# Optimization experiments

Hardware: AMD Instinct MI355X
Metric: run time of the kernel (lower is better)

The kernel has to match this reference:

```python
import jax, jax.numpy as jnp
import numpy as np

EMBED_DIM = 1024
HEAD_SIZE = 64
B, T = 4, 4096


def setup_inputs() -> dict:
    key = jax.random.key(0)
    kx, kq, kk, kv = jax.random.split(key, 4)
    x = jax.random.normal(kx, (B, T, EMBED_DIM), dtype=jnp.float32)
    sw = 1.0 / np.sqrt(EMBED_DIM)  # kaiming-ish init scale for linear weights
    Wq = jax.random.normal(kq, (EMBED_DIM, HEAD_SIZE), dtype=jnp.float32) * sw
    Wk = jax.random.normal(kk, (EMBED_DIM, HEAD_SIZE), dtype=jnp.float32) * sw
    Wv = jax.random.normal(kv, (EMBED_DIM, HEAD_SIZE), dtype=jnp.float32) * sw
    return {"x": x, "Wq": Wq, "Wk": Wk, "Wv": Wv}


def reference(x, Wq, Wk, Wv):
    Bn, Tn, C = x.shape
    q = jnp.einsum('btc,ch->bth', x, Wq)
    k = jnp.einsum('btc,ch->bth', x, Wk)
    v = jnp.einsum('btc,ch->bth', x, Wv)
    # NOTE: original scales by sqrt(C) = sqrt(embed_dim), not sqrt(head_size)
    scale = 1.0 / jnp.sqrt(jnp.asarray(C, dtype=x.dtype))
    wei = jnp.einsum('bth,bsh->bts', q, k) * scale  # [B, T, T]
    causal = jnp.tril(jnp.ones((Tn, Tn), dtype=bool))
    wei = jnp.where(causal, wei, -jnp.inf)
    wei = jax.nn.softmax(wei, axis=-1)
    # dropout p=0.0 (eval mode): identity
    return jnp.einsum('bts,bsh->bth', wei, v)
```

## Files before the change

### kernel.cpp

```cpp
#include <hip/hip_runtime.h>
#include <cstdint>


typedef __bf16 bf16;
typedef __bf16 bf16x4 __attribute__((ext_vector_type(4)));
typedef __bf16 bf16x8 __attribute__((ext_vector_type(8)));
typedef float  f32x4  __attribute__((ext_vector_type(4)));

#define MFMA16(a, b, c) __builtin_amdgcn_mfma_f32_16x16x32_bf16((a), (b), (c), 0, 0, 0)

#if __has_builtin(__builtin_amdgcn_exp2f)
#define EXP2(x) __builtin_amdgcn_exp2f(x)
#else
#define EXP2(x) exp2f(x)
#endif

#define B_SZ 4
#define T_SZ 4096
#define C_SZ 1024
#define H_SZ 64
#define M_SZ (B_SZ * T_SZ)
#define QSCALE (1.4426950408889634f / 32.0f)
#define P_O 8192
#define P_L 128

__device__ __forceinline__ void dma16(const void* g, void* l) {
    __builtin_amdgcn_global_load_lds(
        (const __attribute__((address_space(1))) uint32_t*)(uintptr_t)g,
        (__attribute__((address_space(3))) uint32_t*)(uint32_t)(uintptr_t)l,
        16, 0, 0);
}

__device__ __forceinline__ void pipe_sync() {
    asm volatile("s_waitcnt vmcnt(0)" ::: "memory");
    __builtin_amdgcn_s_barrier();
    __builtin_amdgcn_sched_barrier(0);
}

__global__ __launch_bounds__(256) void wt_prep(
    const float* __restrict__ Wq, const float* __restrict__ Wk,
    const float* __restrict__ Wv, bf16* __restrict__ wt2)
{
    const int n4 = blockIdx.x, t = threadIdx.x;
    const int nbase = n4 * 4;
    const float* W = (nbase < 64) ? Wq : (nbase < 128 ? Wk : Wv);
    const float sc = (nbase < 64) ? QSCALE : 1.0f;
    const int ncol = nbase & 63;
    #pragma unroll
    for (int i = 0; i < 4; ++i) {
        const int k = i * 256 + t;
        const float4 v = *(const float4*)(W + (size_t)k * H_SZ + ncol);
        const float vals[4] = {v.x, v.y, v.z, v.w};
        const size_t base = (size_t)(k >> 6) * 12288 + (size_t)((k >> 5) & 1) * 6144
                          + (size_t)((k >> 3) & 3) * 1536 + (k & 7);
        #pragma unroll
        for (int m = 0; m < 4; ++m)
            wt2[base + (size_t)(nbase + m) * 8] = (bf16)(vals[m] * sc);
    }
}

__global__ __launch_bounds__(256) void qkv_proj(
    const float* __restrict__ x, const bf16* __restrict__ wt2,
    bf16* __restrict__ qw, bf16* __restrict__ kw2, bf16* __restrict__ vtw2)
{
    const int m0 = blockIdx.x * 32;
    const int tid = threadIdx.x;
    const int wave = tid >> 6, lane = tid & 63;
    const int quad = lane >> 4, l15 = lane & 15;
    const int phase = blockIdx.x & 15;

    __shared__ __align__(16) float xs[2 * 4 * 32 * 8];
    __shared__ __align__(16) bf16  ws[2 * 4 * 192 * 8];

    f32x4 acc[2][3] = {};

    const char* xg = (const char*)x
        + (size_t)(m0 + ((tid >> 1) & 31)) * 4096
        + (size_t)((tid >> 6) & 3) * 32 + (size_t)(tid & 1) * 16;
    char* xl = (char*)xs + (size_t)tid * 16;
    const char* wg = (const char*)wt2 + (size_t)tid * 16;
    char* wl = (char*)ws + (size_t)tid * 16;

    for (int s = 0; s < 16; ++s) {
        const size_t se = (size_t)((s + phase) & 15);
        __syncthreads();
        dma16(xg + se * 256, xl);
        dma16(xg + se * 256 + 128, xl + 4096);
        #pragma unroll
        for (int i = 0; i < 6; ++i)
            dma16(wg + se * 24576 + (size_t)i * 4096, wl + (size_t)i * 4096);
        __syncthreads();

        #pragma unroll
        for (int ss = 0; ss < 2; ++ss) {
            bf16x8 a[2];
            #pragma unroll
            for (int mg = 0; mg < 2; ++mg) {
                const float* ap = xs + ss * 1024 + quad * 256 + (mg * 16 + l15) * 8;
                const f32x4 lo = *(const f32x4*)ap;
                const f32x4 hi = *(const f32x4*)(ap + 4);
                a[mg][0] = (bf16)lo[0]; a[mg][1] = (bf16)lo[1];
                a[mg][2] = (bf16)lo[2]; a[mg][3] = (bf16)lo[3];
                a[mg][4] = (bf16)hi[0]; a[mg][5] = (bf16)hi[1];
                a[mg][6] = (bf16)hi[2]; a[mg][7] = (bf16)hi[3];
            }
            #pragma unroll
            for (int i = 0; i < 3; ++i) {
                const int nt = wave * 3 + i;
                const bf16x8 wf = *(const bf16x8*)(ws + ss * 6144 + quad * 1536
                                                   + (nt * 16 + l15) * 8);
                #pragma unroll
                for (int mg = 0; mg < 2; ++mg)
                    acc[mg][i] = MFMA16(a[mg], wf, acc[mg][i]);
            }
        }
    }

    #pragma unroll
    for (int mg = 0; mg < 2; ++mg)
        #pragma unroll
        for (int i = 0; i < 3; ++i) {
            const int n = (wave * 3 + i) * 16 + l15;
            const int which = n >> 6, col = n & 63;
            #pragma unroll
            for (int r = 0; r < 4; ++r) {
                const int t = m0 + mg * 16 + quad * 4 + r;
                const bf16 v = (bf16)acc[mg][i][r];
                if (which == 0) {
                    qw[(size_t)t * H_SZ + col] = v;
                } else if (which == 1) {
                    kw2[(size_t)(t >> 6) * 4096
                        + (size_t)(((col >> 5) << 2) + ((col >> 3) & 3)) * 512
                        + (size_t)(t & 63) * 8 + (col & 7)] = v;
                } else {
                    const int t6 = t & 63;
                    const int p = ((t6 >> 2) & 3) * 8 + (t6 & 3) * 2
                                + ((t6 >> 4) & 1) + (t6 >> 5) * 32;
                    vtw2[(size_t)(t >> 6) * 4096
                         + (size_t)(p >> 3) * 512 + (size_t)col * 8 + (p & 7)] = v;
                }
            }
        }
}

__global__ __launch_bounds__(256) void flash_attn(
    const bf16* __restrict__ qw, const bf16* __restrict__ kw2,
    const bf16* __restrict__ vtw2, bf16* __restrict__ pbuf_o,
    float* __restrict__ pbuf_l)
{
    const int bx = blockIdx.x;
    const int item = (bx & 1) ? (511 - (bx >> 1)) : (bx >> 1);
    const int qt2 = 31 - (item >> 4);
    const int b   = (item >> 2) & 3;
    const int h   = item & 3;
    const int i0  = qt2 * 128;
    const int nkv = qt2 * 2 + 2;

    const int tid = threadIdx.x;
    const int wave = tid >> 6, lane = tid & 63;
    const int quad = lane >> 4, l15 = lane & 15;

    __shared__ __align__(16) bf16 kvs[2][8192];

    bf16x8 aq[2][2];
    #pragma unroll
    for (int mg2 = 0; mg2 < 2; ++mg2) {
        const bf16* qp = qw + ((size_t)b * T_SZ + i0 + wave * 32 + mg2 * 16 + l15) * H_SZ
                       + quad * 8;
        aq[mg2][0] = *(const bf16x8*)qp;
        aq[mg2][1] = *(const bf16x8*)(qp + 32);
    }
    const bf16 onev = (bf16)1.0f;
    const bf16x8 vone = {onev, onev, onev, onev, onev, onev, onev, onev};

    const char* kgb = (const char*)kw2 + (size_t)b * 524288;
    const char* vgb = (const char*)vtw2 + (size_t)b * 524288;

    f32x4 o[2][4] = {};
    f32x4 osum[2] = {};

    auto stage = [&](int jt, int buf) {
        const char* ks = kgb + (size_t)jt * 8192;
        const char* vs = vgb + (size_t)jt * 8192;
        char* dst = (char*)(&kvs[buf][0]) + (size_t)tid * 16;
        dma16(ks + (size_t)tid * 16, dst);
        dma16(ks + 4096 + (size_t)tid * 16, dst + 4096);
        dma16(vs + (size_t)tid * 16, dst + 8192);
        dma16(vs + 4096 + (size_t)tid * 16, dst + 12288);
    };

    if (h < nkv) {
        stage(h, 0);
        pipe_sync();
    }

    int c = 0;
    for (int jt = h; jt < nkv; jt += 4, c ^= 1) {
        if (jt + 4 < nkv) stage(jt + 4, c ^ 1);
        const bf16* kb = &kvs[c][0];
        const bf16* vb = &kvs[c][0] + 4096;

        f32x4 s4t[4][2] = {};
        __builtin_amdgcn_s_setprio(1);
        #pragma unroll
        for (int ct = 0; ct < 4; ++ct) {
            const bf16x8 k0 = *(const bf16x8*)(kb + (0 * 4 + quad) * 512 + (ct * 16 + l15) * 8);
            const bf16x8 k1 = *(const bf16x8*)(kb + (1 * 4 + quad) * 512 + (ct * 16 + l15) * 8);
            #pragma unroll
            for (int mg2 = 0; mg2 < 2; ++mg2) {
                s4t[ct][mg2] = MFMA16(k0, aq[mg2][0], s4t[ct][mg2]);
                s4t[ct][mg2] = MFMA16(k1, aq[mg2][1], s4t[ct][mg2]);
            }
        }
        __builtin_amdgcn_s_setprio(0);

        if (jt >= 2 * qt2) {
            #pragma unroll
            for (int mg2 = 0; mg2 < 2; ++mg2) {
                const int gq = i0 + wave * 32 + mg2 * 16 + l15;
                #pragma unroll
                for (int ct = 0; ct < 4; ++ct) {
                    const int gkv0 = jt * 64 + ct * 16 + quad * 4;
                    #pragma unroll
                    for (int rr = 0; rr < 4; ++rr)
                        if (gkv0 + rr > gq) s4t[ct][mg2][rr] = -3.0e38f;
                }
            }
        }

        bf16x8 pa[2][2];
        #pragma unroll
        for (int mg2 = 0; mg2 < 2; ++mg2)
            #pragma unroll
            for (int j = 0; j < 8; ++j) {
                pa[mg2][0][j] = (bf16)EXP2(s4t[j & 1][mg2][j >> 1]);
                pa[mg2][1][j] = (bf16)EXP2(s4t[2 + (j & 1)][mg2][j >> 1]);
            }

        __builtin_amdgcn_s_setprio(1);
        #pragma unroll
        for (int ht = 0; ht < 4; ++ht) {
            const bf16x8 v0 = *(const bf16x8*)(vb + (0 * 4 + quad) * 512 + (ht * 16 + l15) * 8);
            const bf16x8 v1 = *(const bf16x8*)(vb + (1 * 4 + quad) * 512 + (ht * 16 + l15) * 8);
            #pragma unroll
            for (int mg2 = 0; mg2 < 2; ++mg2) {
                o[mg2][ht] = MFMA16(pa[mg2][0], v0, o[mg2][ht]);
                o[mg2][ht] = MFMA16(pa[mg2][1], v1, o[mg2][ht]);
            }
        }
        #pragma unroll
        for (int mg2 = 0; mg2 < 2; ++mg2) {
            osum[mg2] = MFMA16(pa[mg2][0], vone, osum[mg2]);
            osum[mg2] = MFMA16(pa[mg2][1], vone, osum[mg2]);
        }
        __builtin_amdgcn_s_setprio(0);

        pipe_sync();
    }

    bf16* pb_o = pbuf_o + (size_t)(((b * 32 + qt2) * 4) + h) * P_O;
    float* pb_l = pbuf_l + (size_t)(((b * 32 + qt2) * 4) + h) * P_L;
    #pragma unroll
    for (int mg2 = 0; mg2 < 2; ++mg2) {
        const int L0 = wave * 32 + mg2 * 16 + quad * 4;
        #pragma unroll
        for (int ht = 0; ht < 4; ++ht)
            #pragma unroll
            for (int rr = 0; rr < 4; ++rr)
                pb_o[(L0 + rr) * 64 + ht * 16 + l15] = (bf16)o[mg2][ht][rr];
        if (l15 == 0) {
            #pragma unroll
            for (int rr = 0; rr < 4; ++rr)
                pb_l[L0 + rr] = osum[mg2][rr];
        }
    }
}

__global__ __launch_bounds__(256) void combine(
    const bf16* __restrict__ pbuf_o, const float* __restrict__ pbuf_l,
    float* __restrict__ out)
{
    const int bq2 = blockIdx.x >> 1, tid = threadIdx.x;
    const int row = ((blockIdx.x & 1) << 6) + (tid >> 2);
    const int c0 = (tid & 3) * 16;

    float a[16] = {};
    float l = 0.f;
    #pragma unroll
    for (int h = 0; h < 4; ++h) {
        const bf16* ph = pbuf_o + (size_t)(bq2 * 4 + h) * P_O + row * 64 + c0;
        const bf16x8 v0 = *(const bf16x8*)ph;
        const bf16x8 v1 = *(const bf16x8*)(ph + 8);
        #pragma unroll
        for (int j = 0; j < 8; ++j) {
            a[j]     += (float)v0[j];
            a[8 + j] += (float)v1[j];
        }
        l += pbuf_l[(size_t)(bq2 * 4 + h) * P_L + row];
    }
    const float inv = 1.0f / l;
    float* op = out + ((size_t)bq2 * 128 + row) * 64 + c0;
    #pragma unroll
    for (int g = 0; g < 4; ++g) {
        f32x4 v = {a[g * 4], a[g * 4 + 1], a[g * 4 + 2], a[g * 4 + 3]};
        *(f32x4*)(op + g * 4) = v * inv;
    }
}

extern "C" void kernel_launch(void* const* d_in, const int* in_sizes, int n_in,
                              void* d_out, int out_size, void* d_ws, size_t ws_size,
                              hipStream_t stream) {
    const float* x  = (const float*)d_in[0];
    const float* Wq = (const float*)d_in[1];
    const float* Wk = (const float*)d_in[2];
    const float* Wv = (const float*)d_in[3];

    bf16* qw   = (bf16*)d_ws;
    bf16* kw2  = qw + (size_t)M_SZ * H_SZ;
    bf16* vtw2 = kw2 + (size_t)M_SZ * H_SZ;
    bf16* wt2  = vtw2 + (size_t)M_SZ * H_SZ;
    bf16* pbuf_o = wt2 + 3 * 64 * 1024;
    float* pbuf_l = (float*)(pbuf_o + (size_t)512 * P_O);
    float* out = (float*)d_out;

    wt_prep<<<48, 256, 0, stream>>>(Wq, Wk, Wv, wt2);
    qkv_proj<<<M_SZ / 32, 256, 0, stream>>>(x, wt2, qw, kw2, vtw2);
    flash_attn<<<512, 256, 0, stream>>>(qw, kw2, vtw2, pbuf_o, pbuf_l);
    combine<<<256, 256, 0, stream>>>(pbuf_o, pbuf_l, out);
}
```

Baseline: 142.6 us.

## Double-buffer QKV projection loads and use partial vmcnt waits in attention loop

```diff
diff --git a/kernel.cpp b/kernel.cpp
--- a/kernel.cpp
+++ b/kernel.cpp
@@ -31,11 +31,17 @@
         16, 0, 0);
 }
 
-__device__ __forceinline__ void pipe_sync() {
-    asm volatile("s_waitcnt vmcnt(0)" ::: "memory");
-    __builtin_amdgcn_s_barrier();
-    __builtin_amdgcn_sched_barrier(0);
-}
+#define WAIT_BARRIER(N) do {                                       \
+    asm volatile("s_waitcnt vmcnt(" #N ")" ::: "memory");          \
+    __builtin_amdgcn_s_barrier();                                  \
+    __builtin_amdgcn_sched_barrier(0);                             \
+} while (0)
+
+#define BOT_BARRIER() do {                                         \
+    __builtin_amdgcn_sched_barrier(0);                             \
+    __builtin_amdgcn_s_barrier();                                  \
+    __builtin_amdgcn_sched_barrier(0);                             \
+} while (0)
 
 __global__ __launch_bounds__(256) void wt_prep(
     const float* __restrict__ Wq, const float* __restrict__ Wk,
@@ -69,34 +75,45 @@
     const int quad = lane >> 4, l15 = lane & 15;
     const int phase = blockIdx.x & 15;
 
-    __shared__ __align__(16) float xs[2 * 4 * 32 * 8];
-    __shared__ __align__(16) bf16  ws[2 * 4 * 192 * 8];
+    __shared__ __align__(16) float xs[2][2 * 4 * 32 * 8];
+    __shared__ __align__(16) bf16  ws[2][2 * 4 * 192 * 8];
 
     f32x4 acc[2][3] = {};
 
     const char* xg = (const char*)x
         + (size_t)(m0 + ((tid >> 1) & 31)) * 4096
         + (size_t)((tid >> 6) & 3) * 32 + (size_t)(tid & 1) * 16;
-    char* xl = (char*)xs + (size_t)tid * 16;
     const char* wg = (const char*)wt2 + (size_t)tid * 16;
-    char* wl = (char*)ws + (size_t)tid * 16;
-
-    for (int s = 0; s < 16; ++s) {
+
+    auto stage = [&](int s, int buf) {
         const size_t se = (size_t)((s + phase) & 15);
-        __syncthreads();
+        char* xl = (char*)(&xs[buf][0]) + (size_t)tid * 16;
+        char* wl = (char*)(&ws[buf][0]) + (size_t)tid * 16;
         dma16(xg + se * 256, xl);
         dma16(xg + se * 256 + 128, xl + 4096);
         #pragma unroll
         for (int i = 0; i < 6; ++i)
             dma16(wg + se * 24576 + (size_t)i * 4096, wl + (size_t)i * 4096);
-        __syncthreads();
+    };
+
+    stage(0, 0);
+
+    for (int s = 0; s < 16; ++s) {
+        if (s < 15) {
+            stage(s + 1, (s + 1) & 1);
+            WAIT_BARRIER(8);
+        } else {
+            WAIT_BARRIER(0);
+        }
+        const float* xb = &xs[s & 1][0];
+        const bf16*  wb = &ws[s & 1][0];
 
         #pragma unroll
         for (int ss = 0; ss < 2; ++ss) {
             bf16x8 a[2];
             #pragma unroll
             for (int mg = 0; mg < 2; ++mg) {
-                const float* ap = xs + ss * 1024 + quad * 256 + (mg * 16 + l15) * 8;
+                const float* ap = xb + ss * 1024 + quad * 256 + (mg * 16 + l15) * 8;
                 const f32x4 lo = *(const f32x4*)ap;
                 const f32x4 hi = *(const f32x4*)(ap + 4);
                 a[mg][0] = (bf16)lo[0]; a[mg][1] = (bf16)lo[1];
@@ -107,13 +124,15 @@
             #pragma unroll
             for (int i = 0; i < 3; ++i) {
                 const int nt = wave * 3 + i;
-                const bf16x8 wf = *(const bf16x8*)(ws + ss * 6144 + quad * 1536
+                const bf16x8 wf = *(const bf16x8*)(wb + ss * 6144 + quad * 1536
                                                    + (nt * 16 + l15) * 8);
                 #pragma unroll
                 for (int mg = 0; mg < 2; ++mg)
                     acc[mg][i] = MFMA16(a[mg], wf, acc[mg][i]);
             }
         }
+
+        BOT_BARRIER();
     }
 
     #pragma unroll
@@ -189,14 +208,16 @@
         dma16(vs + 4096 + (size_t)tid * 16, dst + 12288);
     };
 
-    if (h < nkv) {
-        stage(h, 0);
-        pipe_sync();
-    }
+    if (h < nkv) stage(h, 0);
 
     int c = 0;
     for (int jt = h; jt < nkv; jt += 4, c ^= 1) {
-        if (jt + 4 < nkv) stage(jt + 4, c ^ 1);
+        if (jt + 4 < nkv) {
+            stage(jt + 4, c ^ 1);
+            WAIT_BARRIER(4);
+        } else {
+            WAIT_BARRIER(0);
+        }
         const bf16* kb = &kvs[c][0];
         const bf16* vb = &kvs[c][0] + 4096;
 
@@ -255,7 +276,7 @@
         }
         __builtin_amdgcn_s_setprio(0);
 
-        pipe_sync();
+        BOT_BARRIER();
     }
 
     bf16* pb_o = pbuf_o + (size_t)(((b * 32 + qt2) * 4) + h) * P_O;
```

Measured after the change: 141.2 us. No clear change (-1.0%).
